# Kernel tuning notes

Hardware: AMD Instinct MI355X
Metric: run time of the kernel (lower is better)

Reference implementation:

```python
import jax, jax.numpy as jnp
import numpy as np

N_EMBD = 1024  # scale uses C**-0.5 with C = n_embd, as in the original code


def setup_inputs() -> dict:
    key = jax.random.key(0)
    k1, k2, k3, k4 = jax.random.split(key, 4)
    B, T, C, H = 4, 2048, N_EMBD, 64
    x = jax.random.normal(k1, (B, T, C), dtype=jnp.float32)
    # torch Linear weight is [out,in]; we store transposed [in,out] and scale like default init
    s = 1.0 / np.sqrt(C)
    Wq = jax.random.normal(k2, (C, H), dtype=jnp.float32) * s
    Wk = jax.random.normal(k3, (C, H), dtype=jnp.float32) * s
    Wv = jax.random.normal(k4, (C, H), dtype=jnp.float32) * s
    return {"x": x, "Wq": Wq, "Wk": Wk, "Wv": Wv}


def reference(x, Wq, Wk, Wv):
    B, T, C = x.shape
    q = jnp.einsum('btc,ch->bth', x, Wq)
    k = jnp.einsum('btc,ch->bth', x, Wk)
    v = jnp.einsum('btc,ch->bth', x, Wv)
    # kv_cache is None: k,v are the new cache; full causal mask
    scale = C ** -0.5  # NOTE: original scales by n_embd, not head_size
    wei = jnp.einsum('bqh,bkh->bqk', q, k) * scale  # [B,T,T]
    causal = jnp.tril(jnp.ones((T, T), dtype=bool))
    wei = jnp.where(causal, wei, -jnp.inf)
    wei = jax.nn.softmax(wei, axis=-1)
    # dropout: identity (eval mode / deterministic reference)
    out = jnp.einsum('bqk,bkh->bqh', wei, v)
    return (out, k, v)
```

## Files before the change

### kernel.cpp

```cpp
#include <hip/hip_runtime.h>
#include <hip/hip_bf16.h>
#include <stdint.h>


#define NB 4
#define TT 2048
#define CC 1024
#define HH 64
#define NKV (NB * TT * HH)

typedef __attribute__((ext_vector_type(8))) short short8;
typedef __attribute__((ext_vector_type(4))) float f32x4;

__device__ __forceinline__ unsigned short f2bf(float f) {
    union { float f; unsigned int i; } v;
    v.f = f;
    unsigned int r = v.i + 0x7fffu + ((v.i >> 16) & 1u);
    return (unsigned short)(r >> 16);
}
__device__ __forceinline__ unsigned int pkbf2(float a, float b) {
    __hip_bfloat162 h = __float22bfloat162_rn(make_float2(a, b));
    union { __hip_bfloat162 h; unsigned int u; } c;
    c.h = h;
    return c.u;
}

__global__ __launch_bounds__(256) void prep_wb(const float* __restrict__ Wq,
                                               const float* __restrict__ Wk,
                                               const float* __restrict__ Wv,
                                               unsigned short* __restrict__ Wb) {
    int gid = blockIdx.x * 256 + threadIdx.x;
    int j  = gid & 7;
    int l  = (gid >> 3) & 63;
    int kk = (gid >> 9) & 31;
    int s  = gid >> 14;
    int k  = kk * 32 + (l >> 4) * 8 + j;
    int h  = (s & 3) * 16 + (l & 15);
    const float* W = (s >> 2) == 0 ? Wq : (s >> 2) == 1 ? Wk : Wv;
    Wb[gid] = f2bf(W[(size_t)k * HH + h]);
}

#define SC2F 0.0450842200113808f

__global__ __launch_bounds__(512) void qkv_mfma(const float* __restrict__ x,
                                                const unsigned short* __restrict__ Wb,
                                                float* __restrict__ out,
                                                unsigned short* __restrict__ qb,
                                                unsigned short* __restrict__ kb,
                                                unsigned short* __restrict__ vT) {
    __shared__ __align__(16) unsigned short xs[32 * 1024];
    const int t    = threadIdx.x;
    const int wave = t >> 6, lane = t & 63;
    const int n    = lane & 15, quad = lane >> 4;
    const int fw   = wave & 3, rt = wave >> 2;
    const int row0 = blockIdx.x * 32;
    const int b    = row0 >> 11;

    {
        const int tr = t >> 8, tc = t & 255;
#pragma unroll 8
        for (int it = 0; it < 16; ++it) {
            const int i = it * 2 + tr;
            float4 f = *(const float4*)(x + (size_t)(row0 + i) * CC + 4 * tc);
            uint2 u;
            u.x = pkbf2(f.x, f.y);
            u.y = pkbf2(f.z, f.w);
            *(uint2*)&xs[i * 1024 + ((tc ^ ((i & 7) << 1)) << 2)] = u;
        }
    }
    __syncthreads();

    f32x4 acc0 = (f32x4){0.f, 0.f, 0.f, 0.f};
    f32x4 acc1 = acc0, acc2 = acc0;

    const unsigned short* wp = Wb + (size_t)lane * 8;
    const size_t fs = (size_t)32 * 64 * 8;
    const int arow = (rt * 16 + n) * 1024;
    const int axor = (n & 7) << 1;

#pragma unroll 4
    for (int kk = 0; kk < 32; ++kk) {
        short8 a = *(const short8*)&xs[arow + (((kk * 8 + quad * 2) ^ axor) << 2)];
        const unsigned short* wk_ = wp + (size_t)kk * 512;
        short8 b0 = *(const short8*)(wk_ + (size_t)(fw)     * fs);
        short8 b1 = *(const short8*)(wk_ + (size_t)(fw + 4) * fs);
        short8 b2 = *(const short8*)(wk_ + (size_t)(fw + 8) * fs);
        acc0 = __builtin_amdgcn_mfma_f32_16x16x32_bf16(a, b0, acc0, 0, 0, 0);
        acc1 = __builtin_amdgcn_mfma_f32_16x16x32_bf16(a, b1, acc1, 0, 0, 0);
        acc2 = __builtin_amdgcn_mfma_f32_16x16x32_bf16(a, b2, acc2, 0, 0, 0);
    }

    const int h = fw * 16 + n;
    const size_t g0 = (size_t)(row0 + rt * 16 + quad * 4) * HH + h;

    unsigned int uq01 = pkbf2(acc0[0] * SC2F, acc0[1] * SC2F);
    unsigned int uq23 = pkbf2(acc0[2] * SC2F, acc0[3] * SC2F);
    unsigned int uk01 = pkbf2(acc1[0], acc1[1]);
    unsigned int uk23 = pkbf2(acc1[2], acc1[3]);
    qb[g0]          = (unsigned short)uq01;
    qb[g0 + HH]     = (unsigned short)(uq01 >> 16);
    qb[g0 + 2 * HH] = (unsigned short)uq23;
    qb[g0 + 3 * HH] = (unsigned short)(uq23 >> 16);
    kb[g0]          = (unsigned short)uk01;
    kb[g0 + HH]     = (unsigned short)(uk01 >> 16);
    kb[g0 + 2 * HH] = (unsigned short)uk23;
    kb[g0 + 3 * HH] = (unsigned short)(uk23 >> 16);
#pragma unroll
    for (int r = 0; r < 4; ++r) {
        out[NKV + g0 + (size_t)r * HH]     = acc1[r];
        out[2 * NKV + g0 + (size_t)r * HH] = acc2[r];
    }
    uint2 uv;
    uv.x = pkbf2(acc2[0], acc2[1]);
    uv.y = pkbf2(acc2[2], acc2[3]);
    *(uint2*)&vT[(size_t)(b * HH + h) * TT + ((row0 + rt * 16) & 2047) + quad * 4] = uv;
}

__global__ __launch_bounds__(256) void attn_mfma(float* __restrict__ out,
                                                 const unsigned short* __restrict__ qb,
                                                 const unsigned short* __restrict__ kb,
                                                 const unsigned short* __restrict__ vT) {
    __shared__ __align__(16) unsigned short Ps[4][16][72];
    __shared__ float Lb[4][64][4];
    __shared__ float Ob[4][64][16];

    const int t    = threadIdx.x;
    const int wave = t >> 6, lane = t & 63;
    const int n    = lane & 15, quad = lane >> 4;
    const int b    = blockIdx.y;
    const int qt   = (b < 2) ? blockIdx.x : 127 - blockIdx.x;
    const int q0   = qt * 16;

    const unsigned short* qr = qb + (size_t)(b * TT + q0 + n) * HH + quad * 8;
    short8 aq0 = *(const short8*)(qr);
    short8 aq1 = *(const short8*)(qr + 32);

    f32x4 oc[4];
#pragma unroll
    for (int d = 0; d < 4; ++d) oc[d] = (f32x4){0.f, 0.f, 0.f, 0.f};
    float l_[4] = {0.f, 0.f, 0.f, 0.f};

    const int nkt = (q0 >> 6) + 1;

    for (int kt = wave; kt < nkt; kt += 4) {
        const int j0 = kt * 64;

        short8 bk0[4], bk1[4];
#pragma unroll
        for (int s = 0; s < 4; ++s) {
            const unsigned short* kr = kb + (size_t)(b * TT + j0 + s * 16 + n) * HH + quad * 8;
            bk0[s] = *(const short8*)(kr);
            bk1[s] = *(const short8*)(kr + 32);
        }

        short8 bv0[4], bv1[4];
#pragma unroll
        for (int d = 0; d < 4; ++d) {
            const unsigned short* vr = vT + (size_t)(b * HH + d * 16 + n) * TT + j0 + quad * 8;
            bv0[d] = *(const short8*)(vr);
            bv1[d] = *(const short8*)(vr + 32);
        }

        f32x4 sc[4];
#pragma unroll
        for (int s = 0; s < 4; ++s) sc[s] = (f32x4){0.f, 0.f, 0.f, 0.f};
        __builtin_amdgcn_s_setprio(1);
#pragma unroll
        for (int s = 0; s < 4; ++s) {
            sc[s] = __builtin_amdgcn_mfma_f32_16x16x32_bf16(aq0, bk0[s], sc[s], 0, 0, 0);
            sc[s] = __builtin_amdgcn_mfma_f32_16x16x32_bf16(aq1, bk1[s], sc[s], 0, 0, 0);
        }
        __builtin_amdgcn_s_setprio(0);

        float p[4][4];
        if (j0 + 63 <= q0) {
#pragma unroll
            for (int s = 0; s < 4; ++s)
#pragma unroll
                for (int r = 0; r < 4; ++r) {
                    float pe = exp2f(sc[s][r]);
                    p[s][r] = pe;
                    l_[r] += pe;
                }
        } else {
#pragma unroll
            for (int r = 0; r < 4; ++r) {
                const int qrow = q0 + quad * 4 + r;
#pragma unroll
                for (int s = 0; s < 4; ++s) {
                    int krow = j0 + s * 16 + n;
                    float pe = (krow <= qrow) ? exp2f(sc[s][r]) : 0.f;
                    p[s][r] = pe;
                    l_[r] += pe;
                }
            }
        }

#pragma unroll
        for (int s = 0; s < 4; ++s) {
            unsigned int u01 = pkbf2(p[s][0], p[s][1]);
            unsigned int u23 = pkbf2(p[s][2], p[s][3]);
            Ps[wave][quad * 4 + 0][s * 16 + n] = (unsigned short)u01;
            Ps[wave][quad * 4 + 1][s * 16 + n] = (unsigned short)(u01 >> 16);
            Ps[wave][quad * 4 + 2][s * 16 + n] = (unsigned short)u23;
            Ps[wave][quad * 4 + 3][s * 16 + n] = (unsigned short)(u23 >> 16);
        }
        __asm__ volatile("s_waitcnt lgkmcnt(0)" ::: "memory");
        short8 ap0 = *(const short8*)&Ps[wave][n][quad * 8];
        short8 ap1 = *(const short8*)&Ps[wave][n][32 + quad * 8];

        __builtin_amdgcn_s_setprio(1);
#pragma unroll
        for (int d = 0; d < 4; ++d) {
            oc[d] = __builtin_amdgcn_mfma_f32_16x16x32_bf16(ap0, bv0[d], oc[d], 0, 0, 0);
            oc[d] = __builtin_amdgcn_mfma_f32_16x16x32_bf16(ap1, bv1[d], oc[d], 0, 0, 0);
        }
        __builtin_amdgcn_s_setprio(0);
    }

#pragma unroll
    for (int off = 1; off < 16; off <<= 1)
#pragma unroll
        for (int r = 0; r < 4; ++r)
            l_[r] += __shfl_xor(l_[r], off);

#pragma unroll
    for (int r = 0; r < 4; ++r) Lb[wave][lane][r] = l_[r];
#pragma unroll
    for (int d = 0; d < 4; ++d)
#pragma unroll
        for (int r = 0; r < 4; ++r)
            Ob[wave][lane][d * 4 + r] = oc[d][r];
    __syncthreads();

    if (wave == 0) {
#pragma unroll
        for (int r = 0; r < 4; ++r) {
            float ls = Lb[0][lane][r] + Lb[1][lane][r] + Lb[2][lane][r] + Lb[3][lane][r];
            const float inv = 1.f / ls;
#pragma unroll
            for (int d = 0; d < 4; ++d) {
                float o = Ob[0][lane][d * 4 + r] + Ob[1][lane][d * 4 + r] +
                          Ob[2][lane][d * 4 + r] + Ob[3][lane][d * 4 + r];
                out[(size_t)(b * TT + q0 + quad * 4 + r) * HH + d * 16 + n] = o * inv;
            }
        }
    }
}

extern "C" void kernel_launch(void* const* d_in, const int* in_sizes, int n_in,
                              void* d_out, int out_size, void* d_ws, size_t ws_size,
                              hipStream_t stream) {
    const float* x  = (const float*)d_in[0];
    const float* Wq = (const float*)d_in[1];
    const float* Wk = (const float*)d_in[2];
    const float* Wv = (const float*)d_in[3];
    float* out = (float*)d_out;

    char* ws = (char*)d_ws;
    unsigned short* Wb = (unsigned short*)(ws);
    unsigned short* qb = (unsigned short*)(ws + (1u << 20));
    unsigned short* kb = (unsigned short*)(ws + (2u << 20));
    unsigned short* vT = (unsigned short*)(ws + (3u << 20));

    prep_wb<<<768, 256, 0, stream>>>(Wq, Wk, Wv, Wb);
    qkv_mfma<<<256, 512, 0, stream>>>(x, Wb, out, qb, kb, vT);
    attn_mfma<<<dim3(128, 4), 256, 0, stream>>>(out, qb, kb, vT);
}
```

Baseline: 106.9 us.

## Split attention KV loop across two blocks with atomic-flag merge of partials

Adds a second grid dimension so each query tile's key range is split between two blocks, each handling alternating groups of four key tiles. Each block writes partial O and row-sum values to workspace, and the last block to arrive (found by an atomic counter) combines both halves and writes the output. Flags are zeroed in the prep kernel. This doubles the attention grid from 512 blocks to fill more CUs and shorten the long causal tails, in exchange for extra global traffic for partials plus fence and atomic overhead.

```diff
diff --git a/kernel.cpp b/kernel.cpp
--- a/kernel.cpp
+++ b/kernel.cpp
@@ -28,7 +28,12 @@
 __global__ __launch_bounds__(256) void prep_wb(const float* __restrict__ Wq,
                                                const float* __restrict__ Wk,
                                                const float* __restrict__ Wv,
-                                               unsigned short* __restrict__ Wb) {
+                                               unsigned short* __restrict__ Wb,
+                                               unsigned int* __restrict__ flags) {
+    if (blockIdx.x == 0) {
+        flags[threadIdx.x]       = 0u;
+        flags[threadIdx.x + 256] = 0u;
+    }
     int gid = blockIdx.x * 256 + threadIdx.x;
     int j  = gid & 7;
     int l  = (gid >> 3) & 63;
@@ -119,7 +124,10 @@
 __global__ __launch_bounds__(256) void attn_mfma(float* __restrict__ out,
                                                  const unsigned short* __restrict__ qb,
                                                  const unsigned short* __restrict__ kb,
-                                                 const unsigned short* __restrict__ vT) {
+                                                 const unsigned short* __restrict__ vT,
+                                                 unsigned int* __restrict__ flags,
+                                                 float* __restrict__ Lpart,
+                                                 float* __restrict__ Opart) {
     __shared__ __align__(16) unsigned short Ps[4][16][72];
     __shared__ float Lb[4][64][4];
     __shared__ float Ob[4][64][16];
@@ -128,6 +136,7 @@
     const int wave = t >> 6, lane = t & 63;
     const int n    = lane & 15, quad = lane >> 4;
     const int b    = blockIdx.y;
+    const int z    = blockIdx.z;
     const int qt   = (b < 2) ? blockIdx.x : 127 - blockIdx.x;
     const int q0   = qt * 16;
 
@@ -142,7 +151,7 @@
 
     const int nkt = (q0 >> 6) + 1;
 
-    for (int kt = wave; kt < nkt; kt += 4) {
+    for (int kt = z * 4 + wave; kt < nkt; kt += 8) {
         const int j0 = kt * 64;
 
         short8 bk0[4], bk1[4];
@@ -234,15 +243,46 @@
     __syncthreads();
 
     if (wave == 0) {
-#pragma unroll
-        for (int r = 0; r < 4; ++r) {
-            float ls = Lb[0][lane][r] + Lb[1][lane][r] + Lb[2][lane][r] + Lb[3][lane][r];
-            const float inv = 1.f / ls;
-#pragma unroll
-            for (int d = 0; d < 4; ++d) {
-                float o = Ob[0][lane][d * 4 + r] + Ob[1][lane][d * 4 + r] +
-                          Ob[2][lane][d * 4 + r] + Ob[3][lane][d * 4 + r];
-                out[(size_t)(b * TT + q0 + quad * 4 + r) * HH + d * 16 + n] = o * inv;
+        float ls_[4], ob_[4][4];
+#pragma unroll
+        for (int r = 0; r < 4; ++r)
+            ls_[r] = Lb[0][lane][r] + Lb[1][lane][r] + Lb[2][lane][r] + Lb[3][lane][r];
+#pragma unroll
+        for (int d = 0; d < 4; ++d)
+#pragma unroll
+            for (int r = 0; r < 4; ++r)
+                ob_[d][r] = Ob[0][lane][d * 4 + r] + Ob[1][lane][d * 4 + r] +
+                            Ob[2][lane][d * 4 + r] + Ob[3][lane][d * 4 + r];
+
+        const int pidx = b * 128 + qt;
+        float* Op = Opart + ((size_t)pidx * 2 + z) * 1024;
+#pragma unroll
+        for (int r = 0; r < 4; ++r)
+#pragma unroll
+            for (int d = 0; d < 4; ++d)
+                Op[(quad * 4 + r) * 64 + d * 16 + n] = ob_[d][r];
+        if (n == 0) {
+#pragma unroll
+            for (int r = 0; r < 4; ++r)
+                Lpart[(pidx * 2 + z) * 16 + quad * 4 + r] = ls_[r];
+        }
+        __threadfence();
+        unsigned int old = 0;
+        if (lane == 0) old = atomicAdd(&flags[pidx], 1u);
+        old = (unsigned int)__shfl((int)old, 0);
+        if (old == 1) {
+            __threadfence();
+            const float* Oo = Opart + ((size_t)pidx * 2 + (z ^ 1)) * 1024;
+            const float* Lo = Lpart + (pidx * 2 + (z ^ 1)) * 16;
+#pragma unroll
+            for (int r = 0; r < 4; ++r) {
+                const float ls = ls_[r] + Lo[quad * 4 + r];
+                const float inv = 1.f / ls;
+#pragma unroll
+                for (int d = 0; d < 4; ++d) {
+                    float o = ob_[d][r] + Oo[(quad * 4 + r) * 64 + d * 16 + n];
+                    out[(size_t)(b * TT + q0 + quad * 4 + r) * HH + d * 16 + n] = o * inv;
+                }
             }
         }
     }
@@ -262,8 +302,11 @@
     unsigned short* qb = (unsigned short*)(ws + (1u << 20));
     unsigned short* kb = (unsigned short*)(ws + (2u << 20));
     unsigned short* vT = (unsigned short*)(ws + (3u << 20));
-
-    prep_wb<<<768, 256, 0, stream>>>(Wq, Wk, Wv, Wb);
+    unsigned int* flags = (unsigned int*)(ws + (4u << 20));
+    float* Lpart = (float*)(ws + (4u << 20) + 8192);
+    float* Opart = (float*)(ws + (4u << 20) + (128u << 10));
+
+    prep_wb<<<768, 256, 0, stream>>>(Wq, Wk, Wv, Wb, flags);
     qkv_mfma<<<256, 512, 0, stream>>>(x, Wb, out, qb, kb, vT);
-    attn_mfma<<<dim3(128, 4), 256, 0, stream>>>(out, qb, kb, vT);
-}
+    attn_mfma<<<dim3(128, 4, 2), 256, 0, stream>>>(out, qb, kb, vT, flags, Lpart, Opart);
+}
```

Result: slower. 151.8 us (+42.0%).
